# Kernel optimization log

Hardware: AMD Instinct MI355X
Metric: run time of the kernel (lower is better)

## Reference

```python
import jax, jax.numpy as jnp
import numpy as np

N_HEAD = 12


def setup_inputs() -> dict:
    key = jax.random.key(0)
    kx, kq, kk, kv = jax.random.split(key, 4)
    b, n, d = 2, 2048, 768
    x = jax.random.normal(kx, (b, n, d), dtype=jnp.float32)
    # nn.Linear weights stored as [d_out, d_in]; y = x @ W.T (no bias, qkv_bias=False)
    scale = 1.0 / np.sqrt(d)
    Wq = jax.random.normal(kq, (d, d), dtype=jnp.float32) * scale
    Wk = jax.random.normal(kk, (d, d), dtype=jnp.float32) * scale
    Wv = jax.random.normal(kv, (d, d), dtype=jnp.float32) * scale
    return {"x": x, "Wq": Wq, "Wk": Wk, "Wv": Wv}


def reference(x, Wq, Wk, Wv):
    b, n, d = x.shape
    h = N_HEAD
    hd = d // h
    # linear projections (bias=False): x @ W.T, then split heads -> [b, h, n, hd]
    q = (x @ Wq.T).reshape(b, n, h, hd).transpose(0, 2, 1, 3)
    k = (x @ Wk.T).reshape(b, n, h, hd).transpose(0, 2, 1, 3)
    v = (x @ Wv.T).reshape(b, n, h, hd).transpose(0, 2, 1, 3)
    # raw (unscaled!) attention scores, matching the source (no / sqrt(head_dim))
    scores = jnp.einsum('bhqd,bhkd->bhqk', q, k)  # [b, h, n, n]
    causal = jnp.tril(jnp.ones((n, n), dtype=bool))
    scores = jnp.where(causal, scores, -jnp.inf)
    weights = jax.nn.softmax(scores, axis=-1)
    out = jnp.einsum('bhqk,bhkd->bhqd', weights, v)  # [b, h, n, hd]
    return out.transpose(0, 2, 1, 3).reshape(b, n, d)
```

## Files before the change

kernel.cpp:

```cpp
#include <hip/hip_runtime.h>
#include <hip/hip_bf16.h>
#include <stdint.h>

#define Bsz 2
#define NT  2048
#define DM  768
#define NH  12
#define HD  64
#define MT  (Bsz * NT)
#define NCAT (3 * DM)

typedef float    f32x4  __attribute__((ext_vector_type(4)));
typedef float    f32x16 __attribute__((ext_vector_type(16)));
typedef short    s16x8  __attribute__((ext_vector_type(8)));
typedef _Float16 f16x8  __attribute__((ext_vector_type(8)));
typedef int      v2i    __attribute__((ext_vector_type(2)));

#define GLOBAL_AS __attribute__((address_space(1)))
#define SHARED_AS __attribute__((address_space(3)))
#define LOG2E 1.44269504088896f

__device__ inline unsigned short f2h(float f) {
    union { _Float16 h; unsigned short u; } c; c.h = (_Float16)f; return c.u;
}
__device__ inline f16x8 ldh(const short* p) {
    return __builtin_bit_cast(f16x8, *(const s16x8*)p);
}
__device__ inline float exp2i(float x) {
    float r;
    asm("v_exp_f32 %0, %1" : "=v"(r) : "v"(x));
    return r;
}
__device__ inline int cvtpkh(float lo, float hi_) {
    int r;
    asm("v_cvt_pkrtz_f16_f32 %0, %1, %2" : "=v"(r) : "v"(lo), "v"(hi_));
    return r;
}
__device__ inline void plswap(int& a, int& b) {
    v2i r = __builtin_amdgcn_permlane32_swap(a, b, false, false);
    a = r[0]; b = r[1];
}
__device__ inline f16x8 mk8(int a, int b, int c, int d) {
    union { int i[4]; f16x8 v; } u;
    u.i[0] = a; u.i[1] = b; u.i[2] = c; u.i[3] = d;
    return u.v;
}
#define mfma32 __builtin_amdgcn_mfma_f32_32x32x16_f16
#define mfma16 __builtin_amdgcn_mfma_f32_16x16x32_f16


__global__ __launch_bounds__(256) void cvt_x_kernel(const float* __restrict__ x,
                                                    short* __restrict__ xf, int n8) {
    int i = blockIdx.x * blockDim.x + threadIdx.x;
    if (i >= n8) return;
    const float4* p = (const float4*)x + (size_t)i * 2;
    float4 a = p[0], b = p[1];
    float v[8] = {a.x, a.y, a.z, a.w, b.x, b.y, b.z, b.w};
    union { unsigned short s[8]; uint4 q; } H;
#pragma unroll
    for (int j = 0; j < 8; ++j) H.s[j] = f2h(v[j]);
    ((uint4*)xf)[i] = H.q;
}

__global__ __launch_bounds__(256) void cvt_w_kernel(const float* __restrict__ Wq,
                                                    const float* __restrict__ Wk,
                                                    const float* __restrict__ Wv,
                                                    short* __restrict__ Wf, int per8) {
    int i = blockIdx.x * blockDim.x + threadIdx.x;
    if (i >= 3 * per8) return;
    const float* src; int j;
    if (i < per8)          { src = Wq; j = i; }
    else if (i < 2 * per8) { src = Wk; j = i - per8; }
    else                   { src = Wv; j = i - 2 * per8; }
    const float4* p = (const float4*)src + (size_t)j * 2;
    float4 a = p[0], b = p[1];
    float v[8] = {a.x, a.y, a.z, a.w, b.x, b.y, b.z, b.w};
    union { unsigned short s[8]; uint4 q; } H;
#pragma unroll
    for (int t = 0; t < 8; ++t) H.s[t] = f2h(v[t]);
    ((uint4*)Wf)[i] = H.q;
}


#define BM 128
#define BK 32
#define KSTEPS (DM / BK)

__global__ __launch_bounds__(256, 2) void qkv_proj_kernel(
        const short* __restrict__ xf, const short* __restrict__ Wf,
        short* __restrict__ Qf, short* __restrict__ Kf, short* __restrict__ Vf) {
    __shared__ short lds[2][2][BM * BK];

    const int tid = threadIdx.x;
    const int w = tid >> 6, lane = tid & 63;
    const int l15 = lane & 15, lg = lane >> 4;
    const int wr = w >> 1, wc = w & 1;

    const int tile_m = blockIdx.x * BM;
    const int tile_n = blockIdx.y * BM;

    const int arr = w >> 1, hlf = w & 1;
    const int srow = lane >> 2;
    const int scol = (lane & 3) * 8;
    const short* gsrc = (arr == 0) ? xf + (size_t)tile_m * DM
                                   : Wf + (size_t)tile_n * DM;
    const short* gsrc_lane = gsrc + (size_t)(hlf * 64 + srow) * DM + scol;

    f32x4 zero4 = {0.f, 0.f, 0.f, 0.f};
    f32x4 acc[4][4];
#pragma unroll
    for (int i = 0; i < 4; ++i)
#pragma unroll
        for (int j = 0; j < 4; ++j) acc[i][j] = zero4;

    auto stage = [&](int buf, int kt) {
        const short* g = gsrc_lane + kt * BK;
#pragma unroll
        for (int j = 0; j < 4; ++j) {
            __builtin_amdgcn_global_load_lds(
                (const GLOBAL_AS void*)(g + (size_t)j * 16 * DM),
                (SHARED_AS void*)(&lds[buf][arr][(hlf * 64 + j * 16) * BK]),
                16, 0, 0);
        }
    };

    stage(0, 0);
    int cur = 0;
    for (int kt = 0; kt < KSTEPS; ++kt) {
        __syncthreads();
        if (kt + 1 < KSTEPS) stage(cur ^ 1, kt + 1);

        f16x8 a[4], b[4];
#pragma unroll
        for (int f = 0; f < 4; ++f) {
            a[f] = ldh(&lds[cur][0][(wr * 64 + f * 16 + l15) * BK + lg * 8]);
            b[f] = ldh(&lds[cur][1][(wc * 64 + f * 16 + l15) * BK + lg * 8]);
        }
#pragma unroll
        for (int mf = 0; mf < 4; ++mf)
#pragma unroll
            for (int nf = 0; nf < 4; ++nf)
                acc[mf][nf] = mfma16(a[mf], b[nf], acc[mf][nf], 0, 0, 0);
        cur ^= 1;
    }

    const int zq = tile_n / DM;
    const int ncol0 = tile_n % DM;
#pragma unroll
    for (int mf = 0; mf < 4; ++mf) {
#pragma unroll
        for (int nf = 0; nf < 4; ++nf) {
            int col = ncol0 + wc * 64 + nf * 16 + l15;
            int h = col >> 6, dh = col & 63;
            int m0 = tile_m + wr * 64 + mf * 16 + lg * 4;
            int b2 = m0 >> 11, nt0 = m0 & (NT - 1);
            int bh_ = b2 * NH + h;
            if (zq == 2) {
                union { short s[4]; short4 v; } pk;
#pragma unroll
                for (int r = 0; r < 4; ++r) pk.s[r] = (short)f2h(acc[mf][nf][r]);
                *(short4*)&Vf[((size_t)bh_ * HD + dh) * NT + nt0] = pk.v;
            } else {
                short* Hp = (zq == 0) ? Qf : Kf;
                float scl = (zq == 0) ? LOG2E : 1.0f;
#pragma unroll
                for (int r = 0; r < 4; ++r) {
                    size_t oidx = ((size_t)bh_ * NT + nt0 + r) * HD + dh;
                    Hp[oidx] = (short)f2h(acc[mf][nf][r] * scl);
                }
            }
        }
    }
}


#define QB  128
#define KVB 64
#define NQB (NT / QB)
#define SEGT 4
#define SLOTS 72
#define OPA 600

__device__ inline short* op_ptr(short* OpA_, short* OpB_, int g) {
    return (g < OPA) ? OpA_ + (size_t)g * (QB * HD)
                     : OpB_ + (size_t)(g - OPA) * (QB * HD);
}

__global__ __launch_bounds__(256) void attn_part_kernel(const short* __restrict__ Qf,
                                                        const short* __restrict__ Kf,
                                                        const short* __restrict__ Vf,
                                                        short* __restrict__ OpA_,
                                                        short* __restrict__ OpB_,
                                                        float2* __restrict__ ml) {
    int rem = blockIdx.x, a = 0;
    while (rem >= 2 * (a + 1)) { rem -= 2 * (a + 1); ++a; }
    const int qb  = 2 * a + (rem > a);
    const int seg = (rem > a) ? rem - (a + 1) : rem;
    const int bh = blockIdx.y;
    const int g = bh * SLOTS + blockIdx.x;
    const int tid = threadIdx.x;
    const int w = tid >> 6, lane = tid & 63;
    const int l31 = lane & 31, hi = lane >> 5;

    __shared__ __align__(16) short lds[2][2 * 4096];

    const size_t kvoff = (size_t)bh * NT * HD;
    const short* Kfb = Kf + kvoff;
    const short* Vb  = Vf + (size_t)bh * HD * NT;

    const short* sbase[4]; int sstr[4]; int sdof[4];
#pragma unroll
    for (int k = 0; k < 4; ++k) {
        int c = tid + 256 * k;
        int arr = c >> 9, idx = c & 511;
        int row = idx >> 3, ch = idx & 7;
        if (arr == 0) { sbase[k] = Kfb + (size_t)row * HD + ch * 8; sstr[k] = KVB * HD; }
        else          { sbase[k] = Vb + (size_t)row * NT + ch * 8;  sstr[k] = KVB; }
        sdof[k] = arr * 4096 + row * 64 + ((ch ^ (row & 7)) << 3);
    }

    const int q0w   = qb * QB + w * 32;
    const int qg    = q0w + l31;
    const int qmaxw = q0w + 31;

    f16x8 qf[4];
    const size_t qrow = kvoff + (size_t)qg * HD;
#pragma unroll
    for (int c = 0; c < 4; ++c) qf[c] = ldh(Qf + qrow + c * 16 + hi * 8);

    f32x16 o0{}, o1{};
    float m_run = -1e30f, l_run = 0.f;

    const int t0   = seg * SEGT;
    const int tend = min(t0 + SEGT, 2 * qb + 2);

    {
        uint4 ld0[4];
#pragma unroll
        for (int k = 0; k < 4; ++k) ld0[k] = *(const uint4*)(sbase[k] + (size_t)t0 * sstr[k]);
#pragma unroll
        for (int k = 0; k < 4; ++k) *(uint4*)(&lds[0][sdof[k]]) = ld0[k];
    }

    for (int t = t0; t < tend; ++t) {
        __syncthreads();
        const int cur = (t - t0) & 1;
        const int kv0 = t * KVB;
        const bool haveNext = (t + 1 < tend);
        uint4 ldn[4];
        if (haveNext) {
#pragma unroll
            for (int k = 0; k < 4; ++k)
                ldn[k] = *(const uint4*)(sbase[k] + (size_t)(t + 1) * sstr[k]);
        }

        if (kv0 <= qmaxw) {
            const short* Ks = &lds[cur][0];
            const short* Vs = &lds[cur][4096];
#pragma unroll
            for (int c2 = 0; c2 < 2; ++c2) {
                const int kv0c = kv0 + c2 * 32;
                if (kv0c > qmaxw) continue;
                f32x16 S{};
                const int kvr = c2 * 32 + l31;
                const int swb = kvr * 64, sw7 = kvr & 7;
#pragma unroll
                for (int c = 0; c < 4; ++c) {
                    int off = swb + ((((c << 1) + hi) ^ sw7) << 3);
                    S = mfma32(ldh(&Ks[off]), qf[c], S, 0, 0, 0);
                }
                float p[16]; float pmax = -3e38f;
                if (kv0c + 31 > q0w) {
#pragma unroll
                    for (int r = 0; r < 16; ++r) {
                        int kvg = kv0c + (r & 3) + 8 * (r >> 2) + 4 * hi;
                        float sv = (kvg > qg) ? -3e38f : S[r];
                        p[r] = sv;
                        pmax = fmaxf(pmax, sv);
                    }
                } else {
#pragma unroll
                    for (int r = 0; r < 16; ++r) { p[r] = S[r]; pmax = fmaxf(pmax, S[r]); }
                }
                pmax = fmaxf(pmax, __shfl_xor(pmax, 32));
                if (!__all(pmax - m_run <= 11.5416f)) {
                    float mn = fmaxf(m_run, pmax);
                    float al = exp2i(m_run - mn);
                    m_run = mn; l_run *= al;
                    int ai = __builtin_bit_cast(int, al);
#pragma unroll
                    for (int r = 0; r < 16; ++r) {
                        int kr = (r & 3) + 8 * (r >> 2) + 4 * hi;
                        float av = __builtin_bit_cast(float,
                                      __builtin_amdgcn_ds_bpermute(kr << 2, ai));
                        o0[r] *= av; o1[r] *= av;
                    }
                }
                float rs = 0.f;
#pragma unroll
                for (int r = 0; r < 16; ++r) { p[r] = exp2i(p[r] - m_run); rs += p[r]; }
                rs += __shfl_xor(rs, 32);
                l_run += rs;
                int cpk[8];
#pragma unroll
                for (int i = 0; i < 8; ++i) cpk[i] = cvtpkh(p[2 * i], p[2 * i + 1]);
                int a0 = cpk[0], b0 = cpk[2]; plswap(a0, b0);
                int a1 = cpk[1], b1 = cpk[3]; plswap(a1, b1);
                int a2 = cpk[4], b2 = cpk[6]; plswap(a2, b2);
                int a3 = cpk[5], b3 = cpk[7]; plswap(a3, b3);
                f16x8 pf[2] = { mk8(a0, a1, b0, b1), mk8(a2, a3, b2, b3) };
#pragma unroll
                for (int kc = 0; kc < 2; ++kc) {
                    int chunk = c2 * 4 + kc * 2 + hi;
                    int off0 = l31 * 64 + ((chunk ^ (l31 & 7)) << 3);
                    int off1 = (32 + l31) * 64 + ((chunk ^ (l31 & 7)) << 3);
                    o0 = mfma32(pf[kc], ldh(&Vs[off0]), o0, 0, 0, 0);
                    o1 = mfma32(pf[kc], ldh(&Vs[off1]), o1, 0, 0, 0);
                }
            }
        }

        if (haveNext) {
#pragma unroll
            for (int k = 0; k < 4; ++k) *(uint4*)(&lds[cur ^ 1][sdof[k]]) = ldn[k];
        }
    }

    float inv = 1.0f / l_run;
    int ii = __builtin_bit_cast(int, inv);
    short* op = op_ptr(OpA_, OpB_, g);
#pragma unroll
    for (int r = 0; r < 16; ++r) {
        int kr = (r & 3) + 8 * (r >> 2) + 4 * hi;
        float iv = __builtin_bit_cast(float, __builtin_amdgcn_ds_bpermute(kr << 2, ii));
        short* orow = op + (w * 32 + kr) * HD;
        orow[l31]      = (short)f2h(o0[r] * iv);
        orow[32 + l31] = (short)f2h(o1[r] * iv);
    }
    if (hi == 0) {
        float2 v; v.x = m_run; v.y = l_run;
        ml[(size_t)g * QB + w * 32 + l31] = v;
    }
}


__global__ __launch_bounds__(256) void combine_kernel(const short* __restrict__ OpA_,
                                                      const short* __restrict__ OpB_,
                                                      const float2* __restrict__ ml,
                                                      float* __restrict__ out) {
    const int qb = blockIdx.x, bh = blockIdx.y;
    const int b = bh / NH, h = bh % NH;
    const int a = qb >> 1;
    const int nseg = a + 1;
    const int sbase = (a + 1) * (a + (qb & 1));
    const int row = threadIdx.x >> 1;
    const int c0 = (threadIdx.x & 1) * 32;

    float m[8], l[8];
    float M = -3e38f;
    for (int s2 = 0; s2 < nseg; ++s2) {
        float2 t = ml[((size_t)(bh * SLOTS + sbase + s2)) * QB + row];
        m[s2] = t.x; l[s2] = t.y;
        M = fmaxf(M, t.x);
    }
    float wgt[8], L = 0.f;
    for (int s2 = 0; s2 < nseg; ++s2) {
        float e;
        asm("v_exp_f32 %0, %1" : "=v"(e) : "v"(m[s2] - M));
        wgt[s2] = l[s2] * e; L += wgt[s2];
    }
    float invL = 1.0f / L;

    float acc[32];
#pragma unroll
    for (int j = 0; j < 32; ++j) acc[j] = 0.f;
    for (int s2 = 0; s2 < nseg; ++s2) {
        int g = bh * SLOTS + sbase + s2;
        const short* opg = (g < OPA) ? OpA_ + (size_t)g * (QB * HD)
                                     : OpB_ + (size_t)(g - OPA) * (QB * HD);
        const short* oprow = opg + (size_t)row * HD + c0;
        float wg = wgt[s2] * invL;
#pragma unroll
        for (int v = 0; v < 4; ++v) {
            f16x8 d = ldh(oprow + v * 8);
#pragma unroll
            for (int j = 0; j < 8; ++j)
                acc[v * 8 + j] += wg * (float)d[j];
        }
    }
    float* orow = out + ((size_t)(b * NT + qb * QB + row)) * DM + h * HD + c0;
#pragma unroll
    for (int j = 0; j < 32; ++j) orow[j] = acc[j];
}


extern "C" void kernel_launch(void* const* d_in, const int* in_sizes, int n_in,
                              void* d_out, int out_size, void* d_ws, size_t ws_size,
                              hipStream_t stream) {
    const float* x  = (const float*)d_in[0];
    const float* Wq = (const float*)d_in[1];
    const float* Wk = (const float*)d_in[2];
    const float* Wv = (const float*)d_in[3];
    float* outp = (float*)d_out;

    const size_t MD = (size_t)MT * DM;
    const size_t DD = (size_t)DM * DM;

    short* wsp = (short*)d_ws;
    short* xf = wsp;
    short* Wf = xf + MD;
    short* Qf = Wf + 3 * DD;
    short* Kf = Qf + MD;
    short* Vf = Kf + MD;
    short* OpA_ = wsp;
    short* OpB_ = Vf + MD;
    float2* mlp = (float2*)(OpB_ + (size_t)1128 * QB * HD);

    int n8x = (int)(MD / 8);
    cvt_x_kernel<<<dim3((n8x + 255) / 256), 256, 0, stream>>>(x, xf, n8x);
    int per8 = (int)(DD / 8);
    cvt_w_kernel<<<dim3((3 * per8 + 255) / 256), 256, 0, stream>>>(Wq, Wk, Wv, Wf, per8);
    qkv_proj_kernel<<<dim3(MT / BM, NCAT / BM), 256, 0, stream>>>(xf, Wf, Qf, Kf, Vf);
    attn_part_kernel<<<dim3(SLOTS, Bsz * NH), 256, 0, stream>>>(Qf, Kf, Vf, OpA_, OpB_, mlp);
    combine_kernel<<<dim3(NQB, Bsz * NH), 256, 0, stream>>>(OpA_, OpB_, mlp, outp);
}
```

Before: 165.5 us.

## Use larger KV segments and process both 32-key halves per softmax step

Split-KV attention now gives each block up to 8 KV tiles instead of 4, so there are 40 partial slots per head instead of 72. Fewer partial outputs go to memory and the combine step has less to merge. The inner loop now computes scores for both 32-key halves of a 64-key tile before running one online-softmax rescale, which halves the max/rescale/shuffle overhead per tile. The cost is less parallelism (fewer blocks) and higher register pressure from holding two score accumulators.

```diff
diff --git a/kernel.cpp b/kernel.cpp
--- a/kernel.cpp
+++ b/kernel.cpp
@@ -177,14 +177,9 @@
 #define QB  128
 #define KVB 64
 #define NQB (NT / QB)
-#define SEGT 4
-#define SLOTS 72
+#define SEGT 8
+#define SLOTS 40
 #define OPA 600
-
-__device__ inline short* op_ptr(short* OpA_, short* OpB_, int g) {
-    return (g < OPA) ? OpA_ + (size_t)g * (QB * HD)
-                     : OpB_ + (size_t)(g - OPA) * (QB * HD);
-}
 
 __global__ __launch_bounds__(256) void attn_part_kernel(const short* __restrict__ Qf,
                                                         const short* __restrict__ Kf,
@@ -192,12 +187,14 @@
                                                         short* __restrict__ OpA_,
                                                         short* __restrict__ OpB_,
                                                         float2* __restrict__ ml) {
-    int rem = blockIdx.x, a = 0;
-    while (rem >= 2 * (a + 1)) { rem -= 2 * (a + 1); ++a; }
-    const int qb  = 2 * a + (rem > a);
-    const int seg = (rem > a) ? rem - (a + 1) : rem;
+    const int s = blockIdx.x;
+    int qb, seg;
+    if (s < 4)       { qb = s;                  seg = 0; }
+    else if (s < 12) { qb = 4 + ((s - 4) >> 1);   seg = (s - 4) & 1; }
+    else if (s < 24) { qb = 8 + (s - 12) / 3;     seg = (s - 12) % 3; }
+    else             { qb = 12 + ((s - 24) >> 2); seg = (s - 24) & 3; }
     const int bh = blockIdx.y;
-    const int g = bh * SLOTS + blockIdx.x;
+    const int g = bh * SLOTS + s;
     const int tid = threadIdx.x;
     const int w = tid >> 6, lane = tid & 63;
     const int l31 = lane & 31, hi = lane >> 5;
@@ -257,53 +254,69 @@
         if (kv0 <= qmaxw) {
             const short* Ks = &lds[cur][0];
             const short* Vs = &lds[cur][4096];
-#pragma unroll
-            for (int c2 = 0; c2 < 2; ++c2) {
-                const int kv0c = kv0 + c2 * 32;
-                if (kv0c > qmaxw) continue;
-                f32x16 S{};
-                const int kvr = c2 * 32 + l31;
-                const int swb = kvr * 64, sw7 = kvr & 7;
-#pragma unroll
-                for (int c = 0; c < 4; ++c) {
-                    int off = swb + ((((c << 1) + hi) ^ sw7) << 3);
-                    S = mfma32(ldh(&Ks[off]), qf[c], S, 0, 0, 0);
-                }
-                float p[16]; float pmax = -3e38f;
-                if (kv0c + 31 > q0w) {
+            f32x16 Sa{}, Sb{};
+            const int swbA = l31 * 64;
+            const int swbB = (32 + l31) * 64;
+            const int sw7  = l31 & 7;
+#pragma unroll
+            for (int c = 0; c < 4; ++c) {
+                int sh = (((c << 1) + hi) ^ sw7) << 3;
+                Sa = mfma32(ldh(&Ks[swbA + sh]), qf[c], Sa, 0, 0, 0);
+                Sb = mfma32(ldh(&Ks[swbB + sh]), qf[c], Sb, 0, 0, 0);
+            }
+            const bool haveB = (kv0 + 32 <= qmaxw);
+            float pmax = -3e38f;
+            if (kv0 + 31 > q0w) {
+#pragma unroll
+                for (int r = 0; r < 16; ++r) {
+                    int kvg = kv0 + (r & 3) + 8 * (r >> 2) + 4 * hi;
+                    Sa[r] = (kvg > qg) ? -3e38f : Sa[r];
+                    pmax = fmaxf(pmax, Sa[r]);
+                }
+            } else {
+#pragma unroll
+                for (int r = 0; r < 16; ++r) pmax = fmaxf(pmax, Sa[r]);
+            }
+            if (haveB) {
+                if (kv0 + 63 > q0w) {
 #pragma unroll
                     for (int r = 0; r < 16; ++r) {
-                        int kvg = kv0c + (r & 3) + 8 * (r >> 2) + 4 * hi;
-                        float sv = (kvg > qg) ? -3e38f : S[r];
-                        p[r] = sv;
-                        pmax = fmaxf(pmax, sv);
+                        int kvg = kv0 + 32 + (r & 3) + 8 * (r >> 2) + 4 * hi;
+                        Sb[r] = (kvg > qg) ? -3e38f : Sb[r];
+                        pmax = fmaxf(pmax, Sb[r]);
                     }
                 } else {
 #pragma unroll
-                    for (int r = 0; r < 16; ++r) { p[r] = S[r]; pmax = fmaxf(pmax, S[r]); }
-                }
-                pmax = fmaxf(pmax, __shfl_xor(pmax, 32));
-                if (!__all(pmax - m_run <= 11.5416f)) {
-                    float mn = fmaxf(m_run, pmax);
-                    float al = exp2i(m_run - mn);
-                    m_run = mn; l_run *= al;
-                    int ai = __builtin_bit_cast(int, al);
-#pragma unroll
-                    for (int r = 0; r < 16; ++r) {
-                        int kr = (r & 3) + 8 * (r >> 2) + 4 * hi;
-                        float av = __builtin_bit_cast(float,
-                                      __builtin_amdgcn_ds_bpermute(kr << 2, ai));
-                        o0[r] *= av; o1[r] *= av;
-                    }
-                }
-                float rs = 0.f;
-#pragma unroll
-                for (int r = 0; r < 16; ++r) { p[r] = exp2i(p[r] - m_run); rs += p[r]; }
-                rs += __shfl_xor(rs, 32);
-                l_run += rs;
+                    for (int r = 0; r < 16; ++r) pmax = fmaxf(pmax, Sb[r]);
+                }
+            }
+            pmax = fmaxf(pmax, __shfl_xor(pmax, 32));
+            if (!__all(pmax - m_run <= 11.5416f)) {
+                float mn = fmaxf(m_run, pmax);
+                float al = exp2i(m_run - mn);
+                m_run = mn; l_run *= al;
+                int ai = __builtin_bit_cast(int, al);
+#pragma unroll
+                for (int r = 0; r < 16; ++r) {
+                    int kr = (r & 3) + 8 * (r >> 2) + 4 * hi;
+                    float av = __builtin_bit_cast(float,
+                                  __builtin_amdgcn_ds_bpermute(kr << 2, ai));
+                    o0[r] *= av; o1[r] *= av;
+                }
+            }
+            float rs = 0.f;
+#pragma unroll
+            for (int r = 0; r < 16; ++r) { Sa[r] = exp2i(Sa[r] - m_run); rs += Sa[r]; }
+            if (haveB) {
+#pragma unroll
+                for (int r = 0; r < 16; ++r) { Sb[r] = exp2i(Sb[r] - m_run); rs += Sb[r]; }
+            }
+            rs += __shfl_xor(rs, 32);
+            l_run += rs;
+            {
                 int cpk[8];
 #pragma unroll
-                for (int i = 0; i < 8; ++i) cpk[i] = cvtpkh(p[2 * i], p[2 * i + 1]);
+                for (int i = 0; i < 8; ++i) cpk[i] = cvtpkh(Sa[2 * i], Sa[2 * i + 1]);
                 int a0 = cpk[0], b0 = cpk[2]; plswap(a0, b0);
                 int a1 = cpk[1], b1 = cpk[3]; plswap(a1, b1);
                 int a2 = cpk[4], b2 = cpk[6]; plswap(a2, b2);
@@ -311,11 +324,27 @@
                 f16x8 pf[2] = { mk8(a0, a1, b0, b1), mk8(a2, a3, b2, b3) };
 #pragma unroll
                 for (int kc = 0; kc < 2; ++kc) {
-                    int chunk = c2 * 4 + kc * 2 + hi;
-                    int off0 = l31 * 64 + ((chunk ^ (l31 & 7)) << 3);
-                    int off1 = (32 + l31) * 64 + ((chunk ^ (l31 & 7)) << 3);
-                    o0 = mfma32(pf[kc], ldh(&Vs[off0]), o0, 0, 0, 0);
-                    o1 = mfma32(pf[kc], ldh(&Vs[off1]), o1, 0, 0, 0);
+                    int chunk = kc * 2 + hi;
+                    int sh = (chunk ^ (l31 & 7)) << 3;
+                    o0 = mfma32(pf[kc], ldh(&Vs[l31 * 64 + sh]), o0, 0, 0, 0);
+                    o1 = mfma32(pf[kc], ldh(&Vs[(32 + l31) * 64 + sh]), o1, 0, 0, 0);
+                }
+            }
+            if (haveB) {
+                int cpk[8];
+#pragma unroll
+                for (int i = 0; i < 8; ++i) cpk[i] = cvtpkh(Sb[2 * i], Sb[2 * i + 1]);
+                int a0 = cpk[0], b0 = cpk[2]; plswap(a0, b0);
+                int a1 = cpk[1], b1 = cpk[3]; plswap(a1, b1);
+                int a2 = cpk[4], b2 = cpk[6]; plswap(a2, b2);
+                int a3 = cpk[5], b3 = cpk[7]; plswap(a3, b3);
+                f16x8 pf[2] = { mk8(a0, a1, b0, b1), mk8(a2, a3, b2, b3) };
+#pragma unroll
+                for (int kc = 0; kc < 2; ++kc) {
+                    int chunk = 4 + kc * 2 + hi;
+                    int sh = (chunk ^ (l31 & 7)) << 3;
+                    o0 = mfma32(pf[kc], ldh(&Vs[l31 * 64 + sh]), o0, 0, 0, 0);
+                    o1 = mfma32(pf[kc], ldh(&Vs[(32 + l31) * 64 + sh]), o1, 0, 0, 0);
                 }
             }
         }
@@ -328,7 +357,8 @@
 
     float inv = 1.0f / l_run;
     int ii = __builtin_bit_cast(int, inv);
-    short* op = op_ptr(OpA_, OpB_, g);
+    short* op = (g < OPA) ? OpA_ + (size_t)g * (QB * HD)
+                          : OpB_ + (size_t)(g - OPA) * (QB * HD);
 #pragma unroll
     for (int r = 0; r < 16; ++r) {
         int kr = (r & 3) + 8 * (r >> 2) + 4 * hi;
@@ -350,20 +380,20 @@
                                                       float* __restrict__ out) {
     const int qb = blockIdx.x, bh = blockIdx.y;
     const int b = bh / NH, h = bh % NH;
-    const int a = qb >> 1;
-    const int nseg = a + 1;
-    const int sbase = (a + 1) * (a + (qb & 1));
+    const int nseg = (qb >> 2) + 1;
+    const int baseg[4] = {0, 4, 12, 24};
+    const int sbase = baseg[qb >> 2] + (qb & 3) * nseg;
     const int row = threadIdx.x >> 1;
     const int c0 = (threadIdx.x & 1) * 32;
 
-    float m[8], l[8];
+    float m[4], l[4];
     float M = -3e38f;
     for (int s2 = 0; s2 < nseg; ++s2) {
         float2 t = ml[((size_t)(bh * SLOTS + sbase + s2)) * QB + row];
         m[s2] = t.x; l[s2] = t.y;
         M = fmaxf(M, t.x);
     }
-    float wgt[8], L = 0.f;
+    float wgt[4], L = 0.f;
     for (int s2 = 0; s2 < nseg; ++s2) {
         float e;
         asm("v_exp_f32 %0, %1" : "=v"(e) : "v"(m[s2] - M));
@@ -414,7 +444,7 @@
     short* Vf = Kf + MD;
     short* OpA_ = wsp;
     short* OpB_ = Vf + MD;
-    float2* mlp = (float2*)(OpB_ + (size_t)1128 * QB * HD);
+    float2* mlp = (float2*)(OpB_ + (size_t)360 * QB * HD);
 
     int n8x = (int)(MD / 8);
     cvt_x_kernel<<<dim3((n8x + 255) / 256), 256, 0, stream>>>(x, xf, n8x);
```

Result: faster. 161.7 us (-2.3%).
